# Optimization experiments

Measured on AMD Instinct MI355X. Metric: run time of the kernel, lower is better.

## Reference

```python
import jax, jax.numpy as jnp
import numpy as np

D_MODEL = 1024
NHEAD = 16
HEAD_DIM = D_MODEL // NHEAD


def setup_inputs() -> dict:
    key = jax.random.key(0)
    k_x, k_wqkv, k_bqkv, k_wo, k_bo = jax.random.split(key, 5)
    scale_in = 1.0 / np.sqrt(D_MODEL)
    x = jax.random.normal(k_x, (2, 2048, D_MODEL), dtype=jnp.float32)
    # qkv_proj: Linear(d_model, 3*d_model); stored as [in, out] for x @ W
    W_qkv = jax.random.uniform(k_wqkv, (D_MODEL, 3 * D_MODEL), dtype=jnp.float32,
                               minval=-scale_in, maxval=scale_in)
    b_qkv = jax.random.uniform(k_bqkv, (3 * D_MODEL,), dtype=jnp.float32,
                               minval=-scale_in, maxval=scale_in)
    W_out = jax.random.uniform(k_wo, (D_MODEL, D_MODEL), dtype=jnp.float32,
                               minval=-scale_in, maxval=scale_in)
    b_out = jax.random.uniform(k_bo, (D_MODEL,), dtype=jnp.float32,
                               minval=-scale_in, maxval=scale_in)
    return {"x": x, "W_qkv": W_qkv, "b_qkv": b_qkv, "W_out": W_out, "b_out": b_out}


def reference(x, W_qkv, b_qkv, W_out, b_out):
    B, S, _ = x.shape
    qkv = x @ W_qkv + b_qkv                                   # [B,S,3*d_model]
    # Faithful to torch module: reshape to [B,S,H,3*hd], move heads, chunk LAST dim
    qkv = qkv.reshape(B, S, NHEAD, 3 * HEAD_DIM)
    qkv = qkv.transpose(0, 2, 1, 3)                            # [B,H,S,3*hd]
    q, k, v = jnp.split(qkv, 3, axis=-1)                       # each [B,H,S,hd]
    scale = 1.0 / np.sqrt(HEAD_DIM).astype(np.float32)
    attn = jnp.einsum('bhqd,bhkd->bhqk', q, k) * scale         # [B,H,S,S]
    attn = jax.nn.softmax(attn, axis=-1)
    out = jnp.einsum('bhqk,bhkd->bhqd', attn, v)               # [B,H,S,hd]
    out = out.transpose(0, 2, 1, 3).reshape(B, S, D_MODEL)     # [B,S,d_model]
    return out @ W_out + b_out
```

## Files before the change

### kernel.cpp

```cpp
#include <hip/hip_runtime.h>
#include <cmath>

typedef unsigned short u16;
typedef unsigned int u32;
typedef __bf16 bf16x8 __attribute__((ext_vector_type(8)));
typedef float f32x4 __attribute__((ext_vector_type(4)));

#define D_MODEL 1024
#define NHEAD 16
#define HD 64
#define SEQ 2048
#define BATCH 2
#define M_TOK 4096
#define N_QKV 3072

#define Q_SCALE 0.18033688011112042f

__device__ __forceinline__ u16 f2bf(float f) {
    u32 u = __float_as_uint(f);
    u32 r = (u + 0x7fffu + ((u >> 16) & 1u)) >> 16;
    return (u16)r;
}

__device__ __forceinline__ float bf2f(u16 v) {
    return __uint_as_float(((u32)v) << 16);
}

__device__ __forceinline__ float fast_exp2(float x) {
#if __has_builtin(__builtin_amdgcn_exp2f)
    return __builtin_amdgcn_exp2f(x);
#else
    return __exp2f(x);
#endif
}

__device__ __forceinline__ u32 pack_bf(float a, float b) {
#if __has_builtin(__builtin_amdgcn_cvt_pk_bf16_f32)
    typedef __bf16 bf16x2_t __attribute__((ext_vector_type(2)));
    union { bf16x2_t v; u32 u; } c;
    c.v = __builtin_amdgcn_cvt_pk_bf16_f32(a, b);
    return c.u;
#else
    u32 ua = __float_as_uint(a) + 0x8000u;
    u32 ub = __float_as_uint(b) + 0x8000u;
    return __builtin_amdgcn_perm(ub, ua, 0x07060302u);
#endif
}

__device__ __forceinline__ bf16x8 ld_bf8(const u16* p) {
    return *(const bf16x8*)p;
}

__device__ __forceinline__ bf16x8 as_bf8(int4 v) {
    union { int4 i; bf16x8 b; } u; u.i = v; return u.b;
}

__device__ __forceinline__ f32x4 mfma16(bf16x8 a, bf16x8 b, f32x4 c) {
    return __builtin_amdgcn_mfma_f32_16x16x32_bf16(a, b, c, 0, 0, 0);
}

__device__ __forceinline__ void gload_lds16(const u16* g, u16* l) {
    __builtin_amdgcn_global_load_lds(
        (const __attribute__((address_space(1))) void*)g,
        (__attribute__((address_space(3))) void*)l, 16, 0, 0);
}

__device__ __forceinline__ int Gv(int x) {
    int q = x / 192, rm = x - q * 192;
    int e = rm - 128;
    return q * 64 + (e > 0 ? e : 0);
}

__device__ __forceinline__ void transpose_body(
    const float* __restrict__ in, u16* __restrict__ out,
    int rows, int cols, int bx, int by, float (*tile)[33])
{
    int c0 = bx * 32;
    int r0 = by * 32;
    int tx = threadIdx.x & 31;
    int ty = threadIdx.x >> 5;
#pragma unroll
    for (int i = 0; i < 32; i += 8)
        tile[ty + i][tx] = in[(size_t)(r0 + ty + i) * cols + c0 + tx];
    __syncthreads();
#pragma unroll
    for (int i = 0; i < 32; i += 8)
        out[(size_t)(c0 + ty + i) * rows + r0 + tx] = f2bf(tile[tx][ty + i]);
}

__global__ __launch_bounds__(256) void prep_kernel(
    const float* __restrict__ x, u16* __restrict__ Xb,
    const float* __restrict__ Wqkv, u16* __restrict__ Wqkvt,
    const float* __restrict__ Wout, u16* __restrict__ Woutt)
{
    __shared__ float tile[32][33];
    int b = blockIdx.x;
    if (b < 1024) {
        int n4 = M_TOK * D_MODEL / 4;
        int i = b * 256 + threadIdx.x;
        int stride = 1024 * 256;
        for (; i < n4; i += stride) {
            float4 v = ((const float4*)x)[i];
            ushort4 o;
            o.x = f2bf(v.x); o.y = f2bf(v.y); o.z = f2bf(v.z); o.w = f2bf(v.w);
            ((ushort4*)Xb)[i] = o;
        }
    } else if (b < 1024 + 3072) {
        int bb = b - 1024;
        transpose_body(Wqkv, Wqkvt, 1024, 3072, bb % 96, bb / 96, tile);
    } else {
        int bb = b - 4096;
        transpose_body(Wout, Woutt, 1024, 1024, bb % 32, bb / 32, tile);
    }
}

__global__ __launch_bounds__(256) void gemm_qkv_kernel(
    const u16* __restrict__ A, const u16* __restrict__ Bt, const float* __restrict__ bias,
    u16* __restrict__ Qb, u16* __restrict__ Kb, u16* __restrict__ Vp)
{
    __shared__ u16 lA[128 * 32];
    __shared__ u16 lB[128 * 32];
    __shared__ u16 vtile[64 * 132];
    int w = threadIdx.x >> 6, l = threadIdx.x & 63;
    int col = l & 15, quad = l >> 4;
    int wm = w >> 1, wn = w & 1;
    int m0 = blockIdx.x * 128;
    int n0 = blockIdx.y * 128;
    int lrow = l >> 2;
    int lcol = (l & 3) * 8;

    f32x4 acc[4][4] = {};
    for (int k0 = 0; k0 < 1024; k0 += 32) {
        __syncthreads();
#pragma unroll
        for (int i = 0; i < 2; i++) {
            int slab = w * 32 + i * 16;
            gload_lds16(A  + (size_t)(m0 + slab + lrow) * 1024 + k0 + lcol, lA + slab * 32);
            gload_lds16(Bt + (size_t)(n0 + slab + lrow) * 1024 + k0 + lcol, lB + slab * 32);
        }
        __syncthreads();
        bf16x8 af[4], bfr[4];
#pragma unroll
        for (int i = 0; i < 4; i++)
            af[i] = ld_bf8(lA + (wm * 64 + i * 16 + col) * 32 + quad * 8);
#pragma unroll
        for (int j = 0; j < 4; j++)
            bfr[j] = ld_bf8(lB + (wn * 64 + j * 16 + col) * 32 + quad * 8);
#pragma unroll
        for (int i = 0; i < 4; i++)
#pragma unroll
            for (int j = 0; j < 4; j++)
                acc[i][j] = mfma16(af[i], bfr[j], acc[i][j]);
    }

    int s0 = m0 & 2047;
    int bblk = m0 >> 11;
#pragma unroll
    for (int i = 0; i < 4; i++) {
#pragma unroll
        for (int j = 0; j < 4; j++) {
            int cc = n0 + wn * 64 + j * 16 + col;
            int h = cc / 192;
            int within = cc - h * 192;
            int ww = within >> 6;
            int d = within & 63;
            int vloc = Gv(cc) - Gv(n0);
            float bv = bias[cc];
#pragma unroll
            for (int r = 0; r < 4; r++) {
                int sloc = wm * 64 + i * 16 + quad * 4 + r;
                int s = s0 + sloc;
                int bh = bblk * NHEAD + h;
                float val = acc[i][j][r] + bv;
                if (ww == 0)      Qb[(size_t)(bh * SEQ + s) * HD + d] = f2bf(val * Q_SCALE);
                else if (ww == 1) Kb[(size_t)(bh * SEQ + s) * HD + d] = f2bf(val);
                else {
                    int sp = (sloc & ~31) | ((sloc & 12) << 1) | (((sloc >> 4) & 1) << 2) | (sloc & 3);
                    vtile[vloc * 132 + sp] = f2bf(val);
                }
            }
        }
    }
    __syncthreads();
    int vcols = Gv(n0 + 128) - Gv(n0);
    int gbase = Gv(n0);
    for (int c = threadIdx.x; c < vcols * 16; c += 256) {
        int vloc = c >> 4, gi = c & 15;
        int av = gbase + vloc;
        int h = av >> 6, d = av & 63;
        int bh = bblk * NHEAD + h;
        int4 vv = *(const int4*)(vtile + vloc * 132 + gi * 8);
        *(int4*)(Vp + ((size_t)(bh * HD + d)) * SEQ + s0 + gi * 8) = vv;
    }
}

__global__ __launch_bounds__(256, 2) void attn_kernel(
    const u16* __restrict__ Qb, const u16* __restrict__ Kb,
    const u16* __restrict__ Vp, u16* __restrict__ O0,
    u16* __restrict__ O1, float* __restrict__ Lp)
{
    __shared__ u16 kbuf[4][64 * 64];
    __shared__ u16 vbuf[4][64 * 64];
    int wave = threadIdx.x >> 6, lane = threadIdx.x & 63;
    int col = lane & 15, quad = lane >> 4;
    int g = blockIdx.x;
    int xcd = g & 7, slot = g >> 3;
    int bh = xcd * 4 + (slot >> 4);
    int rem = slot & 15;
    int split = rem >> 3;
    int qt = rem & 7;
    int q0 = qt * 256 + wave * 64;
    int kstart = split * 16;

    int srow = lane >> 3;
    int sgrp = (lane & 7) ^ srow;
    const u16* Kt0 = Kb + (size_t)bh * SEQ * HD;
    const u16* Vt0 = Vp + (size_t)bh * HD * SEQ;
    long soffK = (long)srow * HD + sgrp * 8;
    long soffV = (long)srow * SEQ + sgrp * 8;
    int r0 = wave * 16;

    int rbase = col * 64;
    int sw0 = ((quad)     ^ (col & 7)) * 8;
    int sw1 = ((quad + 4) ^ (col & 7)) * 8;

    union { u32 w[4]; int4 i; } onesu;
    onesu.w[0] = onesu.w[1] = onesu.w[2] = onesu.w[3] = 0x3F803F80u;
    bf16x8 ones = as_bf8(onesu.i);

    f32x4 zf = {};

    bf16x8 aq[4][2];
#pragma unroll
    for (int m = 0; m < 4; m++) {
        const u16* qbase = Qb + ((size_t)bh * SEQ + q0 + m * 16 + col) * HD + quad * 8;
        aq[m][0] = ld_bf8(qbase);
        aq[m][1] = ld_bf8(qbase + 32);
    }

    f32x4 o[4][4] = {};
    f32x4 ol[4] = {};

#pragma unroll
    for (int p = 0; p < 2; p++) {
        int kbase = (kstart + p) * 64;
        gload_lds16(Kt0 + (size_t)(kbase + r0) * HD + soffK,      kbuf[p] + r0 * 64);
        gload_lds16(Kt0 + (size_t)(kbase + r0 + 8) * HD + soffK,  kbuf[p] + (r0 + 8) * 64);
        gload_lds16(Vt0 + (size_t)r0 * SEQ + kbase + soffV,       vbuf[p] + r0 * 64);
        gload_lds16(Vt0 + (size_t)(r0 + 8) * SEQ + kbase + soffV, vbuf[p] + (r0 + 8) * 64);
    }

    for (int kt = 0; kt < 16; kt += 2) {
        int pr = (kt >> 1) & 1;
        __syncthreads();
        if (kt + 2 < 16) {
            int npr = pr ^ 1;
#pragma unroll
            for (int p = 0; p < 2; p++) {
                int kbase = (kstart + kt + 2 + p) * 64;
                u16* kd = kbuf[npr * 2 + p];
                u16* vd = vbuf[npr * 2 + p];
                gload_lds16(Kt0 + (size_t)(kbase + r0) * HD + soffK,      kd + r0 * 64);
                gload_lds16(Kt0 + (size_t)(kbase + r0 + 8) * HD + soffK,  kd + (r0 + 8) * 64);
                gload_lds16(Vt0 + (size_t)r0 * SEQ + kbase + soffV,       vd + r0 * 64);
                gload_lds16(Vt0 + (size_t)(r0 + 8) * SEQ + kbase + soffV, vd + (r0 + 8) * 64);
            }
        }
#pragma unroll
        for (int half = 0; half < 2; half++) {
            const u16* kb = kbuf[pr * 2 + half];
            const u16* vb = vbuf[pr * 2 + half];
            bf16x8 kf[4][2];
#pragma unroll
            for (int t = 0; t < 4; t++) {
                kf[t][0] = ld_bf8(kb + t * 1024 + rbase + sw0);
                kf[t][1] = ld_bf8(kb + t * 1024 + rbase + sw1);
            }
            int4 vraw[4][2];
#pragma unroll
            for (int t = 0; t < 4; t++) {
                vraw[t][0] = *(const int4*)(vb + t * 1024 + rbase + sw0);
                vraw[t][1] = *(const int4*)(vb + t * 1024 + rbase + sw1);
            }
#pragma unroll
            for (int m = 0; m < 4; m++) {
                f32x4 sa[4];
                __builtin_amdgcn_s_setprio(1);
#pragma unroll
                for (int t = 0; t < 4; t++) {
                    sa[t] = mfma16(kf[t][0], aq[m][0], zf);
                    sa[t] = mfma16(kf[t][1], aq[m][1], sa[t]);
                }
                __builtin_amdgcn_s_setprio(0);
                int4 pfrag[2];
#pragma unroll
                for (int t = 0; t < 4; t++) {
                    f32x4 p;
#pragma unroll
                    for (int r = 0; r < 4; r++)
                        p[r] = fast_exp2(sa[t][r]);
                    u32 lo = pack_bf(p[0], p[1]);
                    u32 hi = pack_bf(p[2], p[3]);
                    if ((t & 1) == 0) { pfrag[t >> 1].x = (int)lo; pfrag[t >> 1].y = (int)hi; }
                    else              { pfrag[t >> 1].z = (int)lo; pfrag[t >> 1].w = (int)hi; }
                }
                __builtin_amdgcn_s_setprio(1);
#pragma unroll
                for (int t = 0; t < 4; t++)
#pragma unroll
                    for (int h = 0; h < 2; h++)
                        o[m][t] = mfma16(as_bf8(pfrag[h]), as_bf8(vraw[t][h]), o[m][t]);
                ol[m] = mfma16(as_bf8(pfrag[0]), ones, ol[m]);
                ol[m] = mfma16(as_bf8(pfrag[1]), ones, ol[m]);
                __builtin_amdgcn_s_setprio(0);
            }
        }
    }

    u16* Op = split ? O1 : O0;
#pragma unroll
    for (int m = 0; m < 4; m++) {
#pragma unroll
        for (int r = 0; r < 4; r++) {
            int srow2 = q0 + m * 16 + quad * 4 + r;
            if (col == 0)
                Lp[(size_t)split * 32 * SEQ + (size_t)bh * SEQ + srow2] = ol[m][r];
#pragma unroll
            for (int t = 0; t < 4; t++)
                Op[((size_t)bh * SEQ + srow2) * HD + t * 16 + col] = f2bf(o[m][t][r]);
        }
    }
}

__global__ __launch_bounds__(256) void combine_kernel(
    const u16* __restrict__ O0, const u16* __restrict__ O1,
    const float* __restrict__ Lp, u16* __restrict__ At)
{
    int i = blockIdx.x * 256 + threadIdx.x;
    int dg = i & 15;
    int q = (i >> 4) & 2047;
    int bh = i >> 15;
    size_t ob = ((size_t)bh * SEQ + q) * HD + dg * 4;
    ushort4 a = *(const ushort4*)(O0 + ob);
    ushort4 b = *(const ushort4*)(O1 + ob);
    float l = Lp[(size_t)bh * SEQ + q] + Lp[(size_t)32 * SEQ + (size_t)bh * SEQ + q];
    float inv = 1.f / l;
    int bb = bh >> 4, h = bh & 15;
    ushort4 o;
    o.x = f2bf((bf2f(a.x) + bf2f(b.x)) * inv);
    o.y = f2bf((bf2f(a.y) + bf2f(b.y)) * inv);
    o.z = f2bf((bf2f(a.z) + bf2f(b.z)) * inv);
    o.w = f2bf((bf2f(a.w) + bf2f(b.w)) * inv);
    *(ushort4*)(At + ((size_t)(bb * SEQ + q)) * D_MODEL + h * 64 + dg * 4) = o;
}

__global__ __launch_bounds__(256) void gemm_out_kernel(
    const u16* __restrict__ A, const u16* __restrict__ Bt, const float* __restrict__ bias,
    float* __restrict__ out)
{
    __shared__ u16 lA[128 * 32];
    __shared__ u16 lB[128 * 32];
    int w = threadIdx.x >> 6, l = threadIdx.x & 63;
    int col = l & 15, quad = l >> 4;
    int wm = w >> 1, wn = w & 1;
    int m0 = blockIdx.x * 128;
    int n0 = blockIdx.y * 128;
    int lrow = l >> 2;
    int lcol = (l & 3) * 8;

    f32x4 acc[4][4] = {};
    for (int k0 = 0; k0 < 1024; k0 += 32) {
        __syncthreads();
#pragma unroll
        for (int i = 0; i < 2; i++) {
            int slab = w * 32 + i * 16;
            gload_lds16(A  + (size_t)(m0 + slab + lrow) * 1024 + k0 + lcol, lA + slab * 32);
            gload_lds16(Bt + (size_t)(n0 + slab + lrow) * 1024 + k0 + lcol, lB + slab * 32);
        }
        __syncthreads();
        bf16x8 af[4], bfr[4];
#pragma unroll
        for (int i = 0; i < 4; i++)
            af[i] = ld_bf8(lA + (wm * 64 + i * 16 + col) * 32 + quad * 8);
#pragma unroll
        for (int j = 0; j < 4; j++)
            bfr[j] = ld_bf8(lB + (wn * 64 + j * 16 + col) * 32 + quad * 8);
#pragma unroll
        for (int i = 0; i < 4; i++)
#pragma unroll
            for (int j = 0; j < 4; j++)
                acc[i][j] = mfma16(af[i], bfr[j], acc[i][j]);
    }

#pragma unroll
    for (int i = 0; i < 4; i++) {
#pragma unroll
        for (int j = 0; j < 4; j++) {
            int cc = n0 + wn * 64 + j * 16 + col;
            float bv = bias[cc];
#pragma unroll
            for (int r = 0; r < 4; r++) {
                int row = m0 + wm * 64 + i * 16 + quad * 4 + r;
                out[(size_t)row * D_MODEL + cc] = acc[i][j][r] + bv;
            }
        }
    }
}

extern "C" void kernel_launch(void* const* d_in, const int* in_sizes, int n_in,
                              void* d_out, int out_size, void* d_ws, size_t ws_size,
                              hipStream_t stream) {
    const float* x     = (const float*)d_in[0];
    const float* W_qkv = (const float*)d_in[1];
    const float* b_qkv = (const float*)d_in[2];
    const float* W_out = (const float*)d_in[3];
    const float* b_out = (const float*)d_in[4];
    float* out = (float*)d_out;

    char* ws = (char*)d_ws;
    u16* Xb    = (u16*)(ws);
    u16* Wqkvt = (u16*)(ws + (8ull << 20));
    u16* Qb    = (u16*)(ws + (16ull << 20));
    u16* Kb    = (u16*)(ws + (24ull << 20));
    u16* Vp    = (u16*)(ws + (32ull << 20));
    u16* O0    = (u16*)(ws);
    u16* O1    = (u16*)(ws + (8ull << 20));
    float* Lp  = (float*)(ws + (40ull << 20));
    u16* At    = (u16*)(ws + (16ull << 20));
    u16* Woutt = (u16*)(ws + (41ull << 20));

    prep_kernel<<<dim3(5120), 256, 0, stream>>>(x, Xb, W_qkv, Wqkvt, W_out, Woutt);
    gemm_qkv_kernel<<<dim3(32, 24), 256, 0, stream>>>(Xb, Wqkvt, b_qkv, Qb, Kb, Vp);
    attn_kernel<<<dim3(512), 256, 0, stream>>>(Qb, Kb, Vp, O0, O1, Lp);
    combine_kernel<<<dim3(BATCH * NHEAD * SEQ * (HD / 4) / 256), 256, 0, stream>>>(O0, O1, Lp, At);
    gemm_out_kernel<<<dim3(32, 8), 256, 0, stream>>>(At, Woutt, b_out, out);
}
```

Before: 183.2 us.

## Double-buffer LDS tiles in QKV and output projection GEMMs

Both projection GEMMs now use two LDS buffers for the A and B tiles. Each iteration issues the global-to-LDS load for the next K slice before running the MFMAs on the current one, which drops one barrier per iteration and aims to hide global load latency behind compute. The cost is double the LDS for tiles, which may lower occupancy. Correctness relies on the direct-to-LDS loads having completed by the trailing barrier, and whether they can actually overlap depends on how the compiler places waitcnt before that barrier.

```diff
diff --git a/kernel.cpp b/kernel.cpp
--- a/kernel.cpp
+++ b/kernel.cpp
@@ -118,8 +118,8 @@
     const u16* __restrict__ A, const u16* __restrict__ Bt, const float* __restrict__ bias,
     u16* __restrict__ Qb, u16* __restrict__ Kb, u16* __restrict__ Vp)
 {
-    __shared__ u16 lA[128 * 32];
-    __shared__ u16 lB[128 * 32];
+    __shared__ u16 lA[2][128 * 32];
+    __shared__ u16 lB[2][128 * 32];
     __shared__ u16 vtile[64 * 132];
     int w = threadIdx.x >> 6, l = threadIdx.x & 63;
     int col = l & 15, quad = l >> 4;
@@ -129,28 +129,39 @@
     int lrow = l >> 2;
     int lcol = (l & 3) * 8;
 
+#pragma unroll
+    for (int i = 0; i < 2; i++) {
+        int slab = w * 32 + i * 16;
+        gload_lds16(A  + (size_t)(m0 + slab + lrow) * 1024 + lcol, lA[0] + slab * 32);
+        gload_lds16(Bt + (size_t)(n0 + slab + lrow) * 1024 + lcol, lB[0] + slab * 32);
+    }
+    __syncthreads();
+
     f32x4 acc[4][4] = {};
     for (int k0 = 0; k0 < 1024; k0 += 32) {
-        __syncthreads();
-#pragma unroll
-        for (int i = 0; i < 2; i++) {
-            int slab = w * 32 + i * 16;
-            gload_lds16(A  + (size_t)(m0 + slab + lrow) * 1024 + k0 + lcol, lA + slab * 32);
-            gload_lds16(Bt + (size_t)(n0 + slab + lrow) * 1024 + k0 + lcol, lB + slab * 32);
-        }
-        __syncthreads();
+        int cur = (k0 >> 5) & 1;
+        if (k0 + 32 < 1024) {
+            int nxt = cur ^ 1;
+#pragma unroll
+            for (int i = 0; i < 2; i++) {
+                int slab = w * 32 + i * 16;
+                gload_lds16(A  + (size_t)(m0 + slab + lrow) * 1024 + k0 + 32 + lcol, lA[nxt] + slab * 32);
+                gload_lds16(Bt + (size_t)(n0 + slab + lrow) * 1024 + k0 + 32 + lcol, lB[nxt] + slab * 32);
+            }
+        }
         bf16x8 af[4], bfr[4];
 #pragma unroll
         for (int i = 0; i < 4; i++)
-            af[i] = ld_bf8(lA + (wm * 64 + i * 16 + col) * 32 + quad * 8);
+            af[i] = ld_bf8(lA[cur] + (wm * 64 + i * 16 + col) * 32 + quad * 8);
 #pragma unroll
         for (int j = 0; j < 4; j++)
-            bfr[j] = ld_bf8(lB + (wn * 64 + j * 16 + col) * 32 + quad * 8);
+            bfr[j] = ld_bf8(lB[cur] + (wn * 64 + j * 16 + col) * 32 + quad * 8);
 #pragma unroll
         for (int i = 0; i < 4; i++)
 #pragma unroll
             for (int j = 0; j < 4; j++)
                 acc[i][j] = mfma16(af[i], bfr[j], acc[i][j]);
+        __syncthreads();
     }
 
     int s0 = m0 & 2047;
@@ -358,8 +369,8 @@
     const u16* __restrict__ A, const u16* __restrict__ Bt, const float* __restrict__ bias,
     float* __restrict__ out)
 {
-    __shared__ u16 lA[128 * 32];
-    __shared__ u16 lB[128 * 32];
+    __shared__ u16 lA[2][128 * 32];
+    __shared__ u16 lB[2][128 * 32];
     int w = threadIdx.x >> 6, l = threadIdx.x & 63;
     int col = l & 15, quad = l >> 4;
     int wm = w >> 1, wn = w & 1;
@@ -368,28 +379,39 @@
     int lrow = l >> 2;
     int lcol = (l & 3) * 8;
 
+#pragma unroll
+    for (int i = 0; i < 2; i++) {
+        int slab = w * 32 + i * 16;
+        gload_lds16(A  + (size_t)(m0 + slab + lrow) * 1024 + lcol, lA[0] + slab * 32);
+        gload_lds16(Bt + (size_t)(n0 + slab + lrow) * 1024 + lcol, lB[0] + slab * 32);
+    }
+    __syncthreads();
+
     f32x4 acc[4][4] = {};
     for (int k0 = 0; k0 < 1024; k0 += 32) {
-        __syncthreads();
-#pragma unroll
-        for (int i = 0; i < 2; i++) {
-            int slab = w * 32 + i * 16;
-            gload_lds16(A  + (size_t)(m0 + slab + lrow) * 1024 + k0 + lcol, lA + slab * 32);
-            gload_lds16(Bt + (size_t)(n0 + slab + lrow) * 1024 + k0 + lcol, lB + slab * 32);
-        }
-        __syncthreads();
+        int cur = (k0 >> 5) & 1;
+        if (k0 + 32 < 1024) {
+            int nxt = cur ^ 1;
+#pragma unroll
+            for (int i = 0; i < 2; i++) {
+                int slab = w * 32 + i * 16;
+                gload_lds16(A  + (size_t)(m0 + slab + lrow) * 1024 + k0 + 32 + lcol, lA[nxt] + slab * 32);
+                gload_lds16(Bt + (size_t)(n0 + slab + lrow) * 1024 + k0 + 32 + lcol, lB[nxt] + slab * 32);
+            }
+        }
         bf16x8 af[4], bfr[4];
 #pragma unroll
         for (int i = 0; i < 4; i++)
-            af[i] = ld_bf8(lA + (wm * 64 + i * 16 + col) * 32 + quad * 8);
+            af[i] = ld_bf8(lA[cur] + (wm * 64 + i * 16 + col) * 32 + quad * 8);
 #pragma unroll
         for (int j = 0; j < 4; j++)
-            bfr[j] = ld_bf8(lB + (wn * 64 + j * 16 + col) * 32 + quad * 8);
+            bfr[j] = ld_bf8(lB[cur] + (wn * 64 + j * 16 + col) * 32 + quad * 8);
 #pragma unroll
         for (int i = 0; i < 4; i++)
 #pragma unroll
             for (int j = 0; j < 4; j++)
                 acc[i][j] = mfma16(af[i], bfr[j], acc[i][j]);
+        __syncthreads();
     }
 
 #pragma unroll
```

Measured after the change: 186.1 us. No clear change (+1.6%).
